# Kernel optimization log

Hardware: AMD Instinct MI355X
Metric: run time of the kernel (lower is better)

The kernel has to match this reference:

```python
import jax, jax.numpy as jnp
import numpy as np

IN_CH = 512; OUT_CH = 512; NOISE_SIZE = 512; K = 3; A = 0.2
B = 4; H = 32
_G = float(np.sqrt(2.0 / (1.0 + A * A)))                 # leaky_relu gain, a=0.2
CONV_SCALE = _G / float(np.sqrt(IN_CH * K * K))          # equal-lr kaiming scale (fan_in = in_ch*3*3)
MS_SCALE = float(np.sqrt(2.0 / (NOISE_SIZE + IN_CH)))    # equal-lr xavier scale on make_s linear
RGB_SCALE = _G * float(np.sqrt(2.0 / (OUT_CH + 3)))      # equal-lr xavier scale on 1x1 to_rgb


def upsample2x(x):
    # torch F.interpolate(scale_factor=2, mode='bilinear', align_corners=False)
    b, c, h, w = x.shape
    return jax.image.resize(x, (b, c, 2 * h, 2 * w), method='bilinear')


def mod_conv(x, style, weight, bias, ms_w, ms_b, w_scale, demodulate, pad):
    # style -> per-sample input-channel scales s: (B, Cin)
    s = style @ (ms_w.T * MS_SCALE) + ms_b
    Wmod = (weight * w_scale)[None] * s[:, None, :, None, None]   # (B, Cout, Cin, k, k)
    if demodulate:
        d = jax.lax.rsqrt(jnp.sum(Wmod * Wmod, axis=(2, 3, 4)) + 1e-8)
        Wmod = Wmod * d[:, :, None, None, None]
    conv1 = lambda xi, wi: jax.lax.conv_general_dilated(
        xi[None], wi, (1, 1), [(pad, pad), (pad, pad)],
        dimension_numbers=('NCHW', 'OIHW', 'NCHW'))[0]
    y = jax.vmap(conv1)(x, Wmod)                                   # per-sample weights == grouped conv
    return y + bias[None, :, None, None]


def lrelu(x):
    return jnp.where(x >= 0, x, A * x)


def setup_inputs() -> dict:
    key = jax.random.key(0)
    ks = jax.random.split(key, 19)
    r = lambda i, shape: jax.random.normal(ks[i], shape, dtype=jnp.float32)
    return {
        'maps': r(0, (B, IN_CH, H, H)),
        'w': r(1, (B, NOISE_SIZE)),
        'rgb': r(2, (B, 3, H, H)),
        'noise0': r(3, (B, 1, 2 * H, 2 * H)),
        'noise1': r(4, (B, 1, 2 * H, 2 * H)),
        'conv0_w': r(5, (OUT_CH, IN_CH, K, K)),
        'conv0_b': 0.1 * r(6, (OUT_CH,)),
        'ms0_w': r(7, (IN_CH, NOISE_SIZE)),
        'ms0_b': jnp.ones((IN_CH,), jnp.float32),
        'ns0': 0.1 * r(8, (OUT_CH,)),
        'conv1_w': r(9, (OUT_CH, OUT_CH, K, K)),
        'conv1_b': 0.1 * r(10, (OUT_CH,)),
        'ms1_w': r(11, (OUT_CH, NOISE_SIZE)),
        'ms1_b': jnp.ones((OUT_CH,), jnp.float32),
        'ns1': 0.1 * r(12, (OUT_CH,)),
        'rgb_w': r(13, (3, OUT_CH, 1, 1)),
        'rgb_b': 0.1 * r(14, (3,)),
        'msr_w': r(15, (OUT_CH, NOISE_SIZE)),
        'msr_b': jnp.ones((OUT_CH,), jnp.float32),
    }


def reference(maps, w, rgb, noise0, noise1,
              conv0_w, conv0_b, ms0_w, ms0_b, ns0,
              conv1_w, conv1_b, ms1_w, ms1_b, ns1,
              rgb_w, rgb_b, msr_w, msr_b):
    # upsample branch (upsample=True)
    rgb = upsample2x(rgb)
    maps = upsample2x(maps)
    # layer 0: modulated conv -> noise -> leaky relu
    h = mod_conv(maps, w, conv0_w, conv0_b, ms0_w, ms0_b, CONV_SCALE, True, 1)
    h = lrelu(h + ns0[None, :, None, None] * noise0)
    # layer 1
    h = mod_conv(h, w, conv1_w, conv1_b, ms1_w, ms1_b, CONV_SCALE, True, 1)
    h = lrelu(h + ns1[None, :, None, None] * noise1)
    # to_rgb: 1x1 modulated conv, no demodulation
    rgb_out = rgb + mod_conv(h, w, rgb_w, rgb_b, msr_w, msr_b, RGB_SCALE, False, 0)
    return (rgb_out, h)
```

## Files before the change

### kernel.cpp

```cpp
#include <hip/hip_runtime.h>
#include <stdint.h>


#define BATCH 4
#define CH 512
#define NPP 4356
#define HOUT_OFF 49152

static constexpr double G_GAIN = 1.3867504905630728;
static constexpr float CONV_SCALE_F = (float)(G_GAIN / 67.88225099390857);
static constexpr float MS_SCALE_F = 0.044194173824159216f;
static constexpr float RGB_SCALE_F = (float)(G_GAIN * 1.4142135623730951 / 22.693611435820433);

typedef __attribute__((ext_vector_type(8))) short short8;
typedef __attribute__((ext_vector_type(4))) float floatx4;

#define OFF_FLAG   0
#define OFF_S0     256
#define OFF_S1     (OFF_S0 + 8192)
#define OFF_SR     (OFF_S1 + 8192)
#define OFF_D0     (OFF_SR + 8192)
#define OFF_D1     (OFF_D0 + 8192)
#define OFF_B0F    (OFF_D1 + 8192)
#define OFF_B1F    (OFF_B0F + 2048)
#define OFF_NS0F   (OFF_B1F + 2048)
#define OFF_NS1F   (OFF_NS0F + 2048)
#define OFF_RGBBF  (OFF_NS1F + 2048)
#define OFF_WMODR  (OFF_RGBBF + 256)
#define OFF_N0F    (OFF_WMODR + 24576)
#define OFF_N1F    (OFF_N0F + 65536)
#define OFF_WT0    (OFF_N1F + 65536)
#define WT_BYTES   4718592
#define OFF_WT1    (OFF_WT0 + WT_BYTES)
#define OFF_XP0    (OFF_WT1 + WT_BYTES)
#define XP_BYTES   17842176
#define OFF_XP1    (OFF_XP0 + XP_BYTES)

__device__ __forceinline__ float bf2f(unsigned short u) {
  return __uint_as_float(((unsigned int)u) << 16);
}
__device__ __forceinline__ unsigned short f2bf(float f) {
  unsigned int x = __float_as_uint(f);
  unsigned int r = x + 0x7FFFu + ((x >> 16) & 1u);
  return (unsigned short)(r >> 16);
}
__device__ __forceinline__ float ldin(const void* p, long i, int bf) {
  if (bf) return bf2f(((const unsigned short*)p)[i]);
  return ((const float*)p)[i];
}
__device__ __forceinline__ void async_ld16(const void* g, void* l) {
  __builtin_amdgcn_global_load_lds(
      (const __attribute__((address_space(1))) unsigned int*)g,
      (__attribute__((address_space(3))) unsigned int*)l, 16, 0, 0);
}
__device__ __forceinline__ void upw(int o, int n_in, int& lo, int& hi, float& wlo) {
  int k = o >> 1;
  if (o & 1) { lo = k; hi = k + 1; if (hi > n_in - 1) hi = n_in - 1; wlo = 0.75f; }
  else       { lo = k - 1; if (lo < 0) lo = 0; hi = k; wlo = 0.25f; }
}

__global__ void k_flag(const unsigned int* msb, int* flag) {
  if (threadIdx.x == 0 && blockIdx.x == 0)
    *flag = (msb[0] == 0x3F803F80u) ? 1 : 0;
}

__global__ void k_zero(unsigned short* Xp) {
  const int idx = blockIdx.x * 256 + threadIdx.x;
  const int plane = idx / 132;
  const int rem = idx - plane * 132;
  const int row65 = rem >= 66;
  const int col = rem - (row65 ? 66 : 0);
  const short8 z = {0, 0, 0, 0, 0, 0, 0, 0};
  *(short8*)&Xp[((long)plane * NPP + (row65 ? 65 : 0) * 66 + col) * 8] = z;
}

__global__ void k_styles(const void* w, const void* msw0, const void* msb0,
                         const void* msw1, const void* msb1,
                         const void* mswr, const void* msbr,
                         float* s0, float* s1, float* sr, const int* flagp) {
  const int bf = *flagp;
  const int mat = blockIdx.x >> 7, chunk = blockIdx.x & 127;
  const int wv = threadIdx.x >> 6, lane = threadIdx.x & 63;
  const int i = chunk * 4 + wv;
  const void* msw; const void* msb; float* out;
  if (mat == 0)      { msw = msw0; msb = msb0; out = s0; }
  else if (mat == 1) { msw = msw1; msb = msb1; out = s1; }
  else               { msw = mswr; msb = msbr; out = sr; }
  float a[4] = {0.f, 0.f, 0.f, 0.f};
  const int n0 = lane * 8;
  if (bf) {
    short8 m8 = *(const short8*)((const unsigned short*)msw + (long)i * 512 + n0);
    for (int b = 0; b < 4; ++b) {
      short8 w8 = *(const short8*)((const unsigned short*)w + b * 512 + n0);
      float s = 0.f;
      for (int e = 0; e < 8; ++e)
        s += bf2f((unsigned short)m8[e]) * bf2f((unsigned short)w8[e]);
      a[b] = s;
    }
  } else {
    const float* mrow = (const float*)msw + (long)i * 512 + n0;
    float4 m0v = *(const float4*)mrow, m1v = *(const float4*)(mrow + 4);
    for (int b = 0; b < 4; ++b) {
      const float* wr = (const float*)w + b * 512 + n0;
      float4 w0v = *(const float4*)wr, w1v = *(const float4*)(wr + 4);
      a[b] = m0v.x * w0v.x + m0v.y * w0v.y + m0v.z * w0v.z + m0v.w * w0v.w +
             m1v.x * w1v.x + m1v.y * w1v.y + m1v.z * w1v.z + m1v.w * w1v.w;
    }
  }
  for (int off = 1; off < 64; off <<= 1)
    for (int b = 0; b < 4; ++b) a[b] += __shfl_xor(a[b], off, 64);
  if (lane == 0) {
    const float mb = ldin(msb, i, bf);
    for (int b = 0; b < 4; ++b) out[b * 512 + i] = a[b] * MS_SCALE_F + mb;
  }
}

__global__ void k_convert(const void* b0, const void* b1, const void* nv0, const void* nv1,
                          const void* rb, const void* rw, const void* noise0, const void* noise1,
                          float* ob0, float* ob1, float* ons0, float* ons1, float* orb,
                          float* owmr, float* on0, float* on1,
                          const float* sr, const int* flagp) {
  const int bf = *flagp;
  const int t = blockIdx.x * blockDim.x + threadIdx.x;
  const int stride = gridDim.x * blockDim.x;
  if (t < 512) {
    ob0[t] = ldin(b0, t, bf); ob1[t] = ldin(b1, t, bf);
    ons0[t] = ldin(nv0, t, bf); ons1[t] = ldin(nv1, t, bf);
  }
  if (t < 3) orb[t] = ldin(rb, t, bf);
  for (int i = t; i < 16384; i += stride) {
    on0[i] = ldin(noise0, i, bf);
    on1[i] = ldin(noise1, i, bf);
  }
  for (int i = t; i < 4 * 3 * 512; i += stride) {
    int b = i / 1536; int r = i - b * 1536; int c = r >> 9; int ci = r & 511;
    owmr[i] = RGB_SCALE_F * ldin(rw, c * 512 + ci, bf) * sr[b * 512 + ci];
  }
}

__global__ void k_wtd(const void* w0, const void* w1, const float* s0, const float* s1,
                      unsigned short* Wt0, unsigned short* Wt1,
                      float* S0, float* S1, const int* flagp) {
  const int bf = *flagp;
  const int l = blockIdx.x >> 9, co = blockIdx.x & 511;
  const void* w = l ? w1 : w0;
  const float* s = l ? s1 : s0;
  unsigned short* Wt = l ? Wt1 : Wt0;
  float* S = l ? S1 : S0;
  float part[4] = {0.f, 0.f, 0.f, 0.f};
  for (int h = 0; h < 2; ++h) {
    const int ci = threadIdx.x + h * 256;
    const int kb = ci >> 5, q = (ci >> 3) & 3, j = ci & 7;
    const long rbase = ((long)co * 512 + ci) * 9;
    float wsq = 0.f;
    for (int t = 0; t < 9; ++t) {
      float v = ldin(w, rbase + t, bf);
      wsq += v * v;
      Wt[((((long)t * 16 + kb) * 4 + q) * 512 + co) * 8 + j] = f2bf(v);
    }
    for (int b = 0; b < 4; ++b) {
      float sv = s[b * 512 + ci];
      part[b] += sv * sv * wsq;
    }
  }
  __shared__ float red[256 * 4];
  for (int b = 0; b < 4; ++b) red[threadIdx.x * 4 + b] = part[b];
  __syncthreads();
  for (int off = 128; off > 0; off >>= 1) {
    if (threadIdx.x < off)
      for (int b = 0; b < 4; ++b)
        red[threadIdx.x * 4 + b] += red[(threadIdx.x + off) * 4 + b];
    __syncthreads();
  }
  if (threadIdx.x < 4) S[threadIdx.x * 512 + co] = red[threadIdx.x];
}

__global__ void k_upt(const void* maps, const float* s0, unsigned short* Xp0,
                      const int* flagp) {
  const int bf = *flagp;
  const int t = blockIdx.x, kb = blockIdx.y, b = blockIdx.z;
  __shared__ float lds[32][4][32];
  {
    const int ciq = threadIdx.x >> 5;
    const int x = threadIdx.x & 31;
    for (int cc = 0; cc < 4; ++cc) {
      const int ci = cc * 8 + ciq;
      const long cbase = ((long)(b * 512 + kb * 32 + ci)) << 10;
      for (int r = 0; r < 4; ++r) {
        int ir = 2 * t - 1 + r;
        ir = ir < 0 ? 0 : (ir > 31 ? 31 : ir);
        lds[ci][r][x] = ldin(maps, cbase + ir * 32 + x, bf);
      }
    }
  }
  __syncthreads();
  const int q = threadIdx.x >> 6, px = threadIdx.x & 63;
  int xlo, xhi; float wx;
  upw(px, 32, xlo, xhi, wx);
  float sv[8];
  for (int jj = 0; jj < 8; ++jj) sv[jj] = s0[b * 512 + kb * 32 + q * 8 + jj];
  for (int y = 0; y < 4; ++y) {
    const int yg = 4 * t + y;
    int ylo, yhi; float wy;
    upw(yg, 32, ylo, yhi, wy);
    const int rlo = ylo - (2 * t - 1), rhi = yhi - (2 * t - 1);
    short8 pk;
    for (int jj = 0; jj < 8; ++jj) {
      const int ci = q * 8 + jj;
      float vlo = wx * lds[ci][rlo][xlo] + (1.f - wx) * lds[ci][rlo][xhi];
      float vhi = wx * lds[ci][rhi][xlo] + (1.f - wx) * lds[ci][rhi][xhi];
      float v = (wy * vlo + (1.f - wy) * vhi) * sv[jj];
      pk[jj] = (short)f2bf(v);
    }
    *(short8*)&Xp0[((((long)b * 16 + kb) * 4 + q) * NPP + (yg + 1) * 66 + (px + 1)) * 8] = pk;
  }
}

#define MFMA16 __builtin_amdgcn_mfma_f32_16x16x32_bf16
template <int LAYER>
__global__ __launch_bounds__(256, 2) void k_conv(
    const unsigned short* __restrict__ Wt,
    const unsigned short* Xp,
    const float* __restrict__ Ssum,
    const float* __restrict__ bias,
    const float* __restrict__ nsc,
    const float* __restrict__ noise,
    const float* __restrict__ snext,
    unsigned short* XpOut,
    void* dout,
    const int* __restrict__ flagp) {
  __shared__ __align__(16) unsigned short Bl[8192];
  const int idx = blockIdx.x;
  const int mt = idx & 3, b = (idx >> 2) & 3, nt = idx >> 4;
  const int m0 = mt << 7, y0 = nt << 1;
  const int lane = threadIdx.x & 63, wv = threadIdx.x >> 6;
  const int wm = wv >> 1, wn = wv & 1;
  const int q = lane >> 4, l15 = lane & 15;

  const floatx4 vz = {0.f, 0.f, 0.f, 0.f};
  floatx4 c00 = vz, c01 = vz, c02 = vz, c03 = vz;
  floatx4 c10 = vz, c11 = vz, c12 = vz, c13 = vz;
  floatx4 c20 = vz, c21 = vz, c22 = vz, c23 = vz;
  floatx4 c30 = vz, c31 = vz, c32 = vz, c33 = vz;

  const unsigned short* Wbase = Wt + ((long)q * 512 + m0 + wm * 64 + l15) * 8;

  auto issueB2 = [&](int kb, int r0) {
    for (int r = 0; r < 2; ++r) {
      const int row = r0 + r;
      const unsigned short* src =
          Xp + ((((long)b * 16 + kb) * 4 + wv) * NPP + (long)(y0 + row) * 66 + 1 + lane) * 8;
      async_ld16(src, &Bl[((row * 4 + wv) * 64) * 8]);
    }
  };

  short8 aA[3][4], aB[3][4];

#define LOADA(BUF, KB, KY)                                                     \
  {                                                                            \
    _Pragma("unroll") for (int kx = 0; kx < 3; ++kx) {                         \
      const unsigned short* ap =                                               \
          Wbase + ((long)((((KY) * 3 + kx) * 16) + (KB)) << 14);               \
      _Pragma("unroll") for (int i = 0; i < 4; ++i)                            \
          BUF[kx][i] = *(const short8*)(ap + i * 128);                         \
    }                                                                          \
  }

#define WAITBAR() \
  asm volatile("s_waitcnt vmcnt(12) lgkmcnt(0)\n\ts_barrier" ::: "memory")

  const short8 z8 = {0, 0, 0, 0, 0, 0, 0, 0};

#define TAPC(BUF, KX)                                                          \
  {                                                                            \
    short8 aa0 = BUF[KX][0], aa1 = BUF[KX][1], aa2 = BUF[KX][2],               \
           aa3 = BUF[KX][3];                                                   \
    short8 bb0, bb1, bb2, bb3;                                                 \
    {                                                                          \
      int p = 0 * 16 + l15 + (KX);                                             \
      int pc = p < 1 ? 0 : p - 1;                                              \
      bb0 = *(const short8*)&Bl[(sq + pc) * 8];                                \
      if ((KX) == 0) bb0 = (p == 0) ? z8 : bb0;                                \
    }                                                                          \
    bb1 = *(const short8*)&Bl[(sq + 1 * 16 + l15 + (KX)-1) * 8];               \
    bb2 = *(const short8*)&Bl[(sq + 2 * 16 + l15 + (KX)-1) * 8];               \
    {                                                                          \
      int p = 3 * 16 + l15 + (KX);                                             \
      int pc = p > 64 ? 63 : p - 1;                                            \
      bb3 = *(const short8*)&Bl[(sq + pc) * 8];                                \
      if ((KX) == 2) bb3 = (p == 65) ? z8 : bb3;                               \
    }                                                                          \
    c00 = MFMA16(aa0, bb0, c00, 0, 0, 0); c01 = MFMA16(aa0, bb1, c01, 0, 0, 0);\
    c02 = MFMA16(aa0, bb2, c02, 0, 0, 0); c03 = MFMA16(aa0, bb3, c03, 0, 0, 0);\
    c10 = MFMA16(aa1, bb0, c10, 0, 0, 0); c11 = MFMA16(aa1, bb1, c11, 0, 0, 0);\
    c12 = MFMA16(aa1, bb2, c12, 0, 0, 0); c13 = MFMA16(aa1, bb3, c13, 0, 0, 0);\
    c20 = MFMA16(aa2, bb0, c20, 0, 0, 0); c21 = MFMA16(aa2, bb1, c21, 0, 0, 0);\
    c22 = MFMA16(aa2, bb2, c22, 0, 0, 0); c23 = MFMA16(aa2, bb3, c23, 0, 0, 0);\
    c30 = MFMA16(aa3, bb0, c30, 0, 0, 0); c31 = MFMA16(aa3, bb1, c31, 0, 0, 0);\
    c32 = MFMA16(aa3, bb2, c32, 0, 0, 0); c33 = MFMA16(aa3, bb3, c33, 0, 0, 0);\
  }

#define ROUND(CUR, NXT, KY, NKB, NKY, DODMA, DKB, DR0)                         \
  {                                                                            \
    LOADA(NXT, NKB, NKY);                                                      \
    WAITBAR();                                                                 \
    if (DODMA) issueB2((DKB), (DR0));                                          \
    const int sq = ((wn + (KY)) * 4 + q) * 64;                                 \
    TAPC(CUR, 0)                                                               \
    TAPC(CUR, 1)                                                               \
    TAPC(CUR, 2)                                                               \
  }

  issueB2(0, 0);
  LOADA(aA, 0, 0);

#pragma unroll 1
  for (int it = 0; it < 8; ++it) {
    const int kb = it * 2;
    const int kb1 = kb + 1;
    const int kb2 = (kb + 2) & 15;
    ROUND(aA, aB, 0, kb, 1, 1, kb, 2);
    ROUND(aB, aA, 1, kb, 2, 0, 0, 0);
    ROUND(aA, aB, 2, kb1, 0, 1, kb1, 0);
    ROUND(aB, aA, 0, kb1, 1, 1, kb1, 2);
    ROUND(aA, aB, 1, kb1, 2, 0, 0, 0);
    ROUND(aB, aA, 2, kb2, 0, 1, kb2, 0);
  }
#undef ROUND
#undef TAPC
#undef WAITBAR
#undef LOADA

  floatx4 accv[4][4] = {{c00, c01, c02, c03}, {c10, c11, c12, c13},
                        {c20, c21, c22, c23}, {c30, c31, c32, c33}};
  const int bfflag = *flagp;
  const int coB = m0 + (wm << 6) + ((lane >> 4) << 2);
  const int xB = lane & 15;
  const int y = y0 + wn;
  for (int i = 0; i < 4; ++i) {
    const int co = coB + (i << 4);
    float Ds[4], bi[4], nv[4], sx[4];
    for (int r = 0; r < 4; ++r) {
      float Sv = Ssum[b * 512 + co + r];
      Ds[r] = CONV_SCALE_F * rsqrtf(CONV_SCALE_F * CONV_SCALE_F * Sv + 1e-8f);
      bi[r] = bias[co + r];
      nv[r] = nsc[co + r];
      sx[r] = (LAYER == 0) ? snext[b * 512 + co + r] : 0.f;
    }
    for (int j = 0; j < 4; ++j) {
      const int x = (j << 4) + xB;
      const int p = (y << 6) + x;
      const float nz = noise[b * 4096 + p];
      if (LAYER == 0) {
        unsigned long long pk = 0ull;
        for (int r = 0; r < 4; ++r) {
          float v = accv[i][j][r] * Ds[r] + bi[r] + nv[r] * nz;
          v = (v >= 0.f) ? v : 0.2f * v;
          pk |= (unsigned long long)f2bf(v * sx[r]) << (16 * r);
        }
        const int pp = (y + 1) * 66 + (x + 1);
        const long o = ((((long)b * 16 + (co >> 5)) * 4 + ((co >> 3) & 3)) * NPP + pp) * 8 + (co & 7);
        *(unsigned long long*)(XpOut + o) = pk;
      } else {
        for (int r = 0; r < 4; ++r) {
          float v = accv[i][j][r] * Ds[r] + bi[r] + nv[r] * nz;
          v = (v >= 0.f) ? v : 0.2f * v;
          const long o = (((long)(b * 512 + co + r)) << 12) + p;
          if (bfflag) ((unsigned short*)dout)[HOUT_OFF + o] = f2bf(v);
          else        ((float*)dout)[HOUT_OFF + o] = v;
        }
      }
    }
  }
}

__global__ void k_rgb(const void* rgb_in, const float* wmodr, const float* rgbb,
                      void* dout, const int* flagp) {
  const int bf = *flagp;
  const int b = blockIdx.y, p0 = blockIdx.x * 64;
  const int px = threadIdx.x & 63, g = threadIdx.x >> 6;
  const char* hbytes = (const char*)dout + (long)HOUT_OFF * (bf ? 2 : 4);
  float a0 = 0.f, a1 = 0.f, a2 = 0.f;
  const float* wm = wmodr + b * 1536;
  for (int ci = g * 128; ci < g * 128 + 128; ++ci) {
    const long o = (((long)(b * 512 + ci)) << 12) + p0 + px;
    const float hv = bf ? bf2f(((const unsigned short*)hbytes)[o])
                        : ((const float*)hbytes)[o];
    a0 += wm[ci] * hv;
    a1 += wm[512 + ci] * hv;
    a2 += wm[1024 + ci] * hv;
  }
  __shared__ float red[4][3][64];
  red[g][0][px] = a0; red[g][1][px] = a1; red[g][2][px] = a2;
  __syncthreads();
  if (g == 0) {
    const int p = p0 + px;
    const int y = p >> 6, x = p & 63;
    int ylo, yhi, xlo, xhi; float wy, wx;
    upw(y, 32, ylo, yhi, wy);
    upw(x, 32, xlo, xhi, wx);
    for (int c = 0; c < 3; ++c) {
      float s = red[0][c][px] + red[1][c][px] + red[2][c][px] + red[3][c][px];
      const long base = (long)(b * 3 + c) << 10;
      const float v00 = ldin(rgb_in, base + ylo * 32 + xlo, bf);
      const float v01 = ldin(rgb_in, base + ylo * 32 + xhi, bf);
      const float v10 = ldin(rgb_in, base + yhi * 32 + xlo, bf);
      const float v11 = ldin(rgb_in, base + yhi * 32 + xhi, bf);
      const float up = wy * (wx * v00 + (1.f - wx) * v01) +
                       (1.f - wy) * (wx * v10 + (1.f - wx) * v11);
      const float v = up + s + rgbb[c];
      const long o = ((long)(b * 3 + c) << 12) + p;
      if (bf) ((unsigned short*)dout)[o] = f2bf(v);
      else    ((float*)dout)[o] = v;
    }
  }
}

extern "C" void kernel_launch(void* const* d_in, const int* in_sizes, int n_in,
                              void* d_out, int out_size, void* d_ws, size_t ws_size,
                              hipStream_t stream) {
  char* ws = (char*)d_ws;
  int* flag = (int*)(ws + OFF_FLAG);
  float* s0 = (float*)(ws + OFF_S0);
  float* s1 = (float*)(ws + OFF_S1);
  float* sr = (float*)(ws + OFF_SR);
  float* S0 = (float*)(ws + OFF_D0);
  float* S1 = (float*)(ws + OFF_D1);
  float* b0f = (float*)(ws + OFF_B0F);
  float* b1f = (float*)(ws + OFF_B1F);
  float* ns0f = (float*)(ws + OFF_NS0F);
  float* ns1f = (float*)(ws + OFF_NS1F);
  float* rgbbf = (float*)(ws + OFF_RGBBF);
  float* wmodr = (float*)(ws + OFF_WMODR);
  float* n0f = (float*)(ws + OFF_N0F);
  float* n1f = (float*)(ws + OFF_N1F);
  unsigned short* Wt0 = (unsigned short*)(ws + OFF_WT0);
  unsigned short* Wt1 = (unsigned short*)(ws + OFF_WT1);
  unsigned short* Xp0 = (unsigned short*)(ws + OFF_XP0);
  unsigned short* Xp1 = (unsigned short*)(ws + OFF_XP1);

  k_flag<<<1, 64, 0, stream>>>((const unsigned int*)d_in[8], flag);
  k_zero<<<264, 256, 0, stream>>>(Xp0);
  k_styles<<<384, 256, 0, stream>>>(d_in[1], d_in[7], d_in[8], d_in[12], d_in[13],
                                    d_in[17], d_in[18], s0, s1, sr, flag);
  k_convert<<<64, 256, 0, stream>>>(d_in[6], d_in[11], d_in[9], d_in[14], d_in[16],
                                    d_in[15], d_in[3], d_in[4], b0f, b1f, ns0f, ns1f,
                                    rgbbf, wmodr, n0f, n1f, sr, flag);
  k_wtd<<<1024, 256, 0, stream>>>(d_in[5], d_in[10], s0, s1, Wt0, Wt1, S0, S1, flag);
  k_upt<<<dim3(16, 16, 4), 256, 0, stream>>>(d_in[0], s0, Xp0, flag);
  k_conv<0><<<512, 256, 0, stream>>>(Wt0, Xp0, S0, b0f, ns0f, n0f, s1, Xp1,
                                     d_out, flag);
  k_conv<1><<<512, 256, 0, stream>>>(Wt1, Xp1, S1, b1f, ns1f, n1f, s1, Xp1,
                                     d_out, flag);
  k_rgb<<<dim3(64, 4), 256, 0, stream>>>(d_in[2], wmodr, rgbbf, d_out, flag);
  (void)in_sizes; (void)n_in; (void)out_size; (void)ws_size;
}
```

Measured before the change: 292.8 us.

## Double-buffer full input slab per channel block and restructure conv MFMA pipeline

```diff
diff --git a/kernel.cpp b/kernel.cpp
--- a/kernel.cpp
+++ b/kernel.cpp
@@ -229,7 +229,7 @@
     unsigned short* XpOut,
     void* dout,
     const int* __restrict__ flagp) {
-  __shared__ __align__(16) unsigned short Bl[8192];
+  __shared__ __align__(16) unsigned short Bl[16384];
   const int idx = blockIdx.x;
   const int mt = idx & 3, b = (idx >> 2) & 3, nt = idx >> 4;
   const int m0 = mt << 7, y0 = nt << 1;
@@ -243,26 +243,31 @@
   floatx4 c20 = vz, c21 = vz, c22 = vz, c23 = vz;
   floatx4 c30 = vz, c31 = vz, c32 = vz, c33 = vz;
 
-  const unsigned short* Wbase = Wt + ((long)q * 512 + m0 + wm * 64 + l15) * 8;
-
-  auto issueB2 = [&](int kb, int r0) {
-    for (int r = 0; r < 2; ++r) {
-      const int row = r0 + r;
+  const int aoff = (((q << 9) + m0 + (wm << 6) + l15) << 3);
+
+  const int vB   = (wn << 11) + (q << 9) + (l15 << 3);
+  const int vBm1 = (wn << 11) + (q << 9) + ((l15 == 0 ? 0 : l15 - 1) << 3);
+  const int vBp1 = (wn << 11) + (q << 9) + ((l15 == 15 ? 15 : l15 + 1) << 3);
+  const bool e0 = (l15 == 0);
+  const bool e15 = (l15 == 15);
+
+  auto issueB4 = [&](int kbn, int par) {
+    for (int row = 0; row < 4; ++row) {
       const unsigned short* src =
-          Xp + ((((long)b * 16 + kb) * 4 + wv) * NPP + (long)(y0 + row) * 66 + 1 + lane) * 8;
-      async_ld16(src, &Bl[((row * 4 + wv) * 64) * 8]);
+          Xp + ((((long)b * 16 + kbn) * 4 + wv) * NPP + (long)(y0 + row) * 66 + 1 + lane) * 8;
+      async_ld16(src, &Bl[((par << 4) + (row << 2) + wv) << 9]);
     }
   };
 
-  short8 aA[3][4], aB[3][4];
-
-#define LOADA(BUF, KB, KY)                                                     \
+  short8 A0[3][4], A1[3][4];
+
+#define LOADA3(BUF, KB, KY)                                                    \
   {                                                                            \
     _Pragma("unroll") for (int kx = 0; kx < 3; ++kx) {                         \
-      const unsigned short* ap =                                               \
-          Wbase + ((long)((((KY) * 3 + kx) * 16) + (KB)) << 14);               \
+      const unsigned short* rp =                                               \
+          Wt + ((long)((((KY) * 3 + kx) * 16) + (KB)) << 14);                  \
       _Pragma("unroll") for (int i = 0; i < 4; ++i)                            \
-          BUF[kx][i] = *(const short8*)(ap + i * 128);                         \
+          BUF[kx][i] = *(const short8*)(rp + aoff + i * 128);                  \
     }                                                                          \
   }
 
@@ -271,65 +276,101 @@
 
   const short8 z8 = {0, 0, 0, 0, 0, 0, 0, 0};
 
-#define TAPC(BUF, KX)                                                          \
+#define KYPHASE(ABUF, KY, PAR)                                                 \
   {                                                                            \
-    short8 aa0 = BUF[KX][0], aa1 = BUF[KX][1], aa2 = BUF[KX][2],               \
-           aa3 = BUF[KX][3];                                                   \
-    short8 bb0, bb1, bb2, bb3;                                                 \
-    {                                                                          \
-      int p = 0 * 16 + l15 + (KX);                                             \
-      int pc = p < 1 ? 0 : p - 1;                                              \
-      bb0 = *(const short8*)&Bl[(sq + pc) * 8];                                \
-      if ((KX) == 0) bb0 = (p == 0) ? z8 : bb0;                                \
-    }                                                                          \
-    bb1 = *(const short8*)&Bl[(sq + 1 * 16 + l15 + (KX)-1) * 8];               \
-    bb2 = *(const short8*)&Bl[(sq + 2 * 16 + l15 + (KX)-1) * 8];               \
-    {                                                                          \
-      int p = 3 * 16 + l15 + (KX);                                             \
-      int pc = p > 64 ? 63 : p - 1;                                            \
-      bb3 = *(const short8*)&Bl[(sq + pc) * 8];                                \
-      if ((KX) == 2) bb3 = (p == 65) ? z8 : bb3;                               \
-    }                                                                          \
-    c00 = MFMA16(aa0, bb0, c00, 0, 0, 0); c01 = MFMA16(aa0, bb1, c01, 0, 0, 0);\
-    c02 = MFMA16(aa0, bb2, c02, 0, 0, 0); c03 = MFMA16(aa0, bb3, c03, 0, 0, 0);\
-    c10 = MFMA16(aa1, bb0, c10, 0, 0, 0); c11 = MFMA16(aa1, bb1, c11, 0, 0, 0);\
-    c12 = MFMA16(aa1, bb2, c12, 0, 0, 0); c13 = MFMA16(aa1, bb3, c13, 0, 0, 0);\
-    c20 = MFMA16(aa2, bb0, c20, 0, 0, 0); c21 = MFMA16(aa2, bb1, c21, 0, 0, 0);\
-    c22 = MFMA16(aa2, bb2, c22, 0, 0, 0); c23 = MFMA16(aa2, bb3, c23, 0, 0, 0);\
-    c30 = MFMA16(aa3, bb0, c30, 0, 0, 0); c31 = MFMA16(aa3, bb1, c31, 0, 0, 0);\
-    c32 = MFMA16(aa3, bb2, c32, 0, 0, 0); c33 = MFMA16(aa3, bb3, c33, 0, 0, 0);\
-  }
-
-#define ROUND(CUR, NXT, KY, NKB, NKY, DODMA, DKB, DR0)                         \
+    const int bo = (PAR)*8192 + (KY)*2048;                                     \
+    short8 b00 = *(const short8*)&Bl[vBm1 + bo];                               \
+    short8 b01 = *(const short8*)&Bl[vB + bo + 120];                           \
+    short8 b02 = *(const short8*)&Bl[vB + bo + 248];                           \
+    short8 b03 = *(const short8*)&Bl[vB + bo + 376];                           \
+    short8 b10 = *(const short8*)&Bl[vB + bo];                                 \
+    short8 b11 = *(const short8*)&Bl[vB + bo + 128];                           \
+    short8 b12 = *(const short8*)&Bl[vB + bo + 256];                           \
+    short8 b13 = *(const short8*)&Bl[vB + bo + 384];                           \
+    short8 b20 = *(const short8*)&Bl[vB + bo + 8];                             \
+    short8 b21 = *(const short8*)&Bl[vB + bo + 136];                           \
+    short8 b22 = *(const short8*)&Bl[vB + bo + 264];                           \
+    short8 b23 = *(const short8*)&Bl[vBp1 + bo + 384];                         \
+    b00 = e0 ? z8 : b00;                                                       \
+    b23 = e15 ? z8 : b23;                                                      \
+    __builtin_amdgcn_s_setprio(1);                                             \
+    c00 = MFMA16(ABUF[0][0], b00, c00, 0, 0, 0);                               \
+    c01 = MFMA16(ABUF[0][0], b01, c01, 0, 0, 0);                               \
+    c02 = MFMA16(ABUF[0][0], b02, c02, 0, 0, 0);                               \
+    c03 = MFMA16(ABUF[0][0], b03, c03, 0, 0, 0);                               \
+    c10 = MFMA16(ABUF[0][1], b00, c10, 0, 0, 0);                               \
+    c11 = MFMA16(ABUF[0][1], b01, c11, 0, 0, 0);                               \
+    c12 = MFMA16(ABUF[0][1], b02, c12, 0, 0, 0);                               \
+    c13 = MFMA16(ABUF[0][1], b03, c13, 0, 0, 0);                               \
+    c20 = MFMA16(ABUF[0][2], b00, c20, 0, 0, 0);                               \
+    c21 = MFMA16(ABUF[0][2], b01, c21, 0, 0, 0);                               \
+    c22 = MFMA16(ABUF[0][2], b02, c22, 0, 0, 0);                               \
+    c23 = MFMA16(ABUF[0][2], b03, c23, 0, 0, 0);                               \
+    c30 = MFMA16(ABUF[0][3], b00, c30, 0, 0, 0);                               \
+    c31 = MFMA16(ABUF[0][3], b01, c31, 0, 0, 0);                               \
+    c32 = MFMA16(ABUF[0][3], b02, c32, 0, 0, 0);                               \
+    c33 = MFMA16(ABUF[0][3], b03, c33, 0, 0, 0);                               \
+    c00 = MFMA16(ABUF[1][0], b10, c00, 0, 0, 0);                               \
+    c01 = MFMA16(ABUF[1][0], b11, c01, 0, 0, 0);                               \
+    c02 = MFMA16(ABUF[1][0], b12, c02, 0, 0, 0);                               \
+    c03 = MFMA16(ABUF[1][0], b13, c03, 0, 0, 0);                               \
+    c10 = MFMA16(ABUF[1][1], b10, c10, 0, 0, 0);                               \
+    c11 = MFMA16(ABUF[1][1], b11, c11, 0, 0, 0);                               \
+    c12 = MFMA16(ABUF[1][1], b12, c12, 0, 0, 0);                               \
+    c13 = MFMA16(ABUF[1][1], b13, c13, 0, 0, 0);                               \
+    c20 = MFMA16(ABUF[1][2], b10, c20, 0, 0, 0);                               \
+    c21 = MFMA16(ABUF[1][2], b11, c21, 0, 0, 0);                               \
+    c22 = MFMA16(ABUF[1][2], b12, c22, 0, 0, 0);                               \
+    c23 = MFMA16(ABUF[1][2], b13, c23, 0, 0, 0);                               \
+    c30 = MFMA16(ABUF[1][3], b10, c30, 0, 0, 0);                               \
+    c31 = MFMA16(ABUF[1][3], b11, c31, 0, 0, 0);                               \
+    c32 = MFMA16(ABUF[1][3], b12, c32, 0, 0, 0);                               \
+    c33 = MFMA16(ABUF[1][3], b13, c33, 0, 0, 0);                               \
+    c00 = MFMA16(ABUF[2][0], b20, c00, 0, 0, 0);                               \
+    c01 = MFMA16(ABUF[2][0], b21, c01, 0, 0, 0);                               \
+    c02 = MFMA16(ABUF[2][0], b22, c02, 0, 0, 0);                               \
+    c03 = MFMA16(ABUF[2][0], b23, c03, 0, 0, 0);                               \
+    c10 = MFMA16(ABUF[2][1], b20, c10, 0, 0, 0);                               \
+    c11 = MFMA16(ABUF[2][1], b21, c11, 0, 0, 0);                               \
+    c12 = MFMA16(ABUF[2][1], b22, c12, 0, 0, 0);                               \
+    c13 = MFMA16(ABUF[2][1], b23, c13, 0, 0, 0);                               \
+    c20 = MFMA16(ABUF[2][2], b20, c20, 0, 0, 0);                               \
+    c21 = MFMA16(ABUF[2][2], b21, c21, 0, 0, 0);                               \
+    c22 = MFMA16(ABUF[2][2], b22, c22, 0, 0, 0);                               \
+    c23 = MFMA16(ABUF[2][2], b23, c23, 0, 0, 0);                               \
+    c30 = MFMA16(ABUF[2][3], b20, c30, 0, 0, 0);                               \
+    c31 = MFMA16(ABUF[2][3], b21, c31, 0, 0, 0);                               \
+    c32 = MFMA16(ABUF[2][3], b22, c32, 0, 0, 0);                               \
+    c33 = MFMA16(ABUF[2][3], b23, c33, 0, 0, 0);                               \
+    __builtin_amdgcn_s_setprio(0);                                             \
+  }
+
+#define KBROUND(PAR, BUFE, BUFO, KB)                                           \
   {                                                                            \
-    LOADA(NXT, NKB, NKY);                                                      \
     WAITBAR();                                                                 \
-    if (DODMA) issueB2((DKB), (DR0));                                          \
-    const int sq = ((wn + (KY)) * 4 + q) * 64;                                 \
-    TAPC(CUR, 0)                                                               \
-    TAPC(CUR, 1)                                                               \
-    TAPC(CUR, 2)                                                               \
-  }
-
-  issueB2(0, 0);
-  LOADA(aA, 0, 0);
+    issueB4(((KB) + 1) & 15, (PAR) ^ 1);                                       \
+    KYPHASE(BUFE, 0, PAR);                                                     \
+    LOADA3(BUFE, (KB), 2);                                   \
+    KYPHASE(BUFO, 1, PAR);                                                     \
+    LOADA3(BUFO, ((KB) + 1) & 15, 0);                        \
+    KYPHASE(BUFE, 2, PAR);                                                     \
+    LOADA3(BUFE, ((KB) + 1) & 15, 1); \
+  }
+
+  issueB4(0, 0);
+  LOADA3(A0, 0, 0);
+  LOADA3(A1, 0, 1);
 
 #pragma unroll 1
   for (int it = 0; it < 8; ++it) {
     const int kb = it * 2;
-    const int kb1 = kb + 1;
-    const int kb2 = (kb + 2) & 15;
-    ROUND(aA, aB, 0, kb, 1, 1, kb, 2);
-    ROUND(aB, aA, 1, kb, 2, 0, 0, 0);
-    ROUND(aA, aB, 2, kb1, 0, 1, kb1, 0);
-    ROUND(aB, aA, 0, kb1, 1, 1, kb1, 2);
-    ROUND(aA, aB, 1, kb1, 2, 0, 0, 0);
-    ROUND(aB, aA, 2, kb2, 0, 1, kb2, 0);
-  }
-#undef ROUND
-#undef TAPC
+    KBROUND(0, A0, A1, kb);
+    KBROUND(1, A1, A0, kb + 1);
+  }
+#undef KBROUND
+#undef KYPHASE
 #undef WAITBAR
-#undef LOADA
+#undef LOADA3
 
   floatx4 accv[4][4] = {{c00, c01, c02, c03}, {c10, c11, c12, c13},
                         {c20, c21, c22, c23}, {c30, c31, c32, c33}};
```

Measured after the change: 890.2 us. 204% more time.
